# Optimization experiments

Hardware: AMD Instinct MI355X
Metric: run time of the kernel (lower is better)

## Reference

```python
import jax, jax.numpy as jnp
import numpy as np
from jax import lax

BN_EPS = 1e-5


def _zpool(x, axis):
    # stack (mean, max) over `axis` as 2 channels -> [N, 2, A, B]
    return jnp.stack([jnp.mean(x, axis=axis), jnp.max(x, axis=axis)], axis=1)


def _gate(p2, conv_w, conv_b, bn_w, bn_b, bn_rm, bn_rv, i):
    # p2: [N, 2, A, B]; 7x7 conv (2->1, pad 3) + scalar BN + relu + sigmoid
    y = lax.conv_general_dilated(
        p2, conv_w, window_strides=(1, 1), padding=[(3, 3), (3, 3)],
        dimension_numbers=("NCHW", "OIHW", "NCHW"))[:, 0] + conv_b[0]  # [N, A, B]
    y = (y - bn_rm[i]) * lax.rsqrt(bn_rv[i] + BN_EPS) * bn_w[i] + bn_b[i]
    return jax.nn.sigmoid(jnp.maximum(y, 0.0))


def setup_inputs() -> dict:
    key = jax.random.key(0)
    ks = jax.random.split(key, 7)
    N, C, H, W = 256, 2048, 7, 7
    return {
        "x": jax.random.normal(ks[0], (N, C, H, W), dtype=jnp.float32),
        "conv_w": jax.random.normal(ks[1], (1, 2, 7, 7), dtype=jnp.float32) * 0.1,
        "conv_b": jax.random.normal(ks[2], (1,), dtype=jnp.float32) * 0.1,
        "bn_w": jax.random.normal(ks[3], (3,), dtype=jnp.float32),
        "bn_b": jax.random.normal(ks[4], (3,), dtype=jnp.float32),
        "bn_rm": jax.random.normal(ks[5], (3,), dtype=jnp.float32) * 0.1,
        "bn_rv": jax.random.uniform(ks[6], (3,), dtype=jnp.float32),
    }


def reference(x, conv_w, conv_b, bn_w, bn_b, bn_rm, bn_rv):
    # x: [N, C, 7, 7]
    g_hw = _gate(_zpool(x, 1), conv_w, conv_b, bn_w, bn_b, bn_rm, bn_rv, 0)  # [N, 7, 7]
    g_ch = _gate(_zpool(x, 3), conv_w, conv_b, bn_w, bn_b, bn_rm, bn_rv, 1)  # [N, C, 7] indexed by h
    g_cw = _gate(_zpool(x, 2), conv_w, conv_b, bn_w, bn_b, bn_rm, bn_rv, 2)  # [N, C, 7] indexed by w
    gate = (g_hw[:, None, :, :] + g_ch[:, :, :, None] + g_cw[:, :, None, :]) * (1.0 / 3.0)
    return x * gate
```

## Files before the change

kernel.cpp:

```cpp
#include <hip/hip_runtime.h>

#define N_ 256
#define C_ 2048
#define HW_ 49
#define CPB 64
#define NCC 32
#define NCHUNK 8


__global__ __launch_bounds__(256) void k_pool_gate(const float* __restrict__ x,
    const float* __restrict__ cw, const float* __restrict__ cb,
    const float* __restrict__ bnw, const float* __restrict__ bnb,
    const float* __restrict__ bnrm, const float* __restrict__ bnrv,
    float* __restrict__ psum, float* __restrict__ pmax,
    float* __restrict__ gch_g, float* __restrict__ gcw_g) {
  const int bc = blockIdx.x, n = blockIdx.y;
  const int t = threadIdx.x;

  __shared__ __align__(16) float sx[3584];
  __shared__ __align__(16) float pool_lo[4 * 264 * 4];
  __shared__ __align__(16) float pool_hi[4 * 264 * 4];
  __shared__ float part_s[HW_][5];
  __shared__ float part_m[HW_][5];
  __shared__ __align__(16) float s_w[112];

  if (t < 112) {
    int i2w = t / 56, rem = t % 56, p = rem / 8, q = rem % 8;
    s_w[t] = (q < 7) ? cw[i2w * 49 + p * 7 + q] : 0.f;
  }

  float sm = 0.f, mx = -3.4e38f;
  const int hwp = t / 5, sp = t % 5;

  const float4* xv = (const float4*)(x + ((size_t)n * C_ + (size_t)bc * 256) * HW_);
  float4* sv = (float4*)sx;
  #pragma unroll
  for (int pass = 0; pass < 4; ++pass) {
    for (int v = t; v < 784; v += 256) sv[v] = xv[pass * 784 + v];
    __syncthreads();
    if (t < 245) {
      #pragma unroll
      for (int j = 0; j < 13; ++j) {
        int c = sp * 13 + j;
        if (c < CPB) { float a = sx[c * HW_ + hwp]; sm += a; mx = fmaxf(mx, a); }
      }
    }
    for (int i = t; i < 448; i += 256) {
      int lc = i / 7, k = i % 7;
      int base = lc * HW_;
      float s1 = 0.f, m1 = -3.4e38f, s2 = 0.f, m2 = -3.4e38f;
      #pragma unroll
      for (int j = 0; j < 7; ++j) {
        float a = sx[base + k * 7 + j]; s1 += a; m1 = fmaxf(m1, a);
        float b = sx[base + j * 7 + k]; s2 += b; m2 = fmaxf(m2, b);
      }
      int pc = pass * 64 + 3 + lc;
      int kk = k & 3;
      float* pb = (k < 4) ? pool_lo : pool_hi;
      pb[(0 * 264 + pc) * 4 + kk] = s1 * (1.f / 7.f);
      pb[(1 * 264 + pc) * 4 + kk] = m1;
      pb[(2 * 264 + pc) * 4 + kk] = s2 * (1.f / 7.f);
      pb[(3 * 264 + pc) * 4 + kk] = m2;
    }
    __syncthreads();
  }

  if (t < 42) {
    int hc = t / 7, k = t % 7;
    int pc = (hc < 3) ? hc : 259 + (hc - 3);
    int c = bc * 256 - 3 + pc;
    float s1 = 0.f, m1 = 0.f, s2 = 0.f, m2 = 0.f;
    if (c >= 0 && c < C_) {
      m1 = -3.4e38f; m2 = -3.4e38f;
      const float* xp = x + ((size_t)n * C_ + c) * HW_;
      #pragma unroll
      for (int j = 0; j < 7; ++j) {
        float a = xp[k * 7 + j]; s1 += a; m1 = fmaxf(m1, a);
        float b = xp[j * 7 + k]; s2 += b; m2 = fmaxf(m2, b);
      }
      s1 *= (1.f / 7.f); s2 *= (1.f / 7.f);
    }
    int kk = k & 3;
    float* pb = (k < 4) ? pool_lo : pool_hi;
    pb[(0 * 264 + pc) * 4 + kk] = s1;
    pb[(1 * 264 + pc) * 4 + kk] = m1;
    pb[(2 * 264 + pc) * 4 + kk] = s2;
    pb[(3 * 264 + pc) * 4 + kk] = m2;
  }
  if (t < 245) { part_s[hwp][sp] = sm; part_m[hwp][sp] = mx; }
  __syncthreads();

  if (t < HW_) {
    float s2 = 0.f, m2 = -3.4e38f;
    #pragma unroll
    for (int k = 0; k < 5; ++k) { s2 += part_s[t][k]; m2 = fmaxf(m2, part_m[t][k]); }
    size_t o = ((size_t)n * NCHUNK + bc) * HW_ + t;
    psum[o] = s2; pmax[o] = m2;
  }

  const float cb0 = cb[0];
  const float sc1 = bnw[1] * rsqrtf(bnrv[1] + 1e-5f), rm1 = bnrm[1], sh1 = bnb[1];
  const float sc2 = bnw[2] * rsqrtf(bnrv[2] + 1e-5f), rm2 = bnrm[2], sh2 = bnb[2];
  float g0[7] = {0, 0, 0, 0, 0, 0, 0};
  float g1[7] = {0, 0, 0, 0, 0, 0, 0};
  #pragma unroll
  for (int f = 0; f < 4; ++f) {
    const float* Wb = s_w + (f & 1) * 56;
    #pragma unroll
    for (int p = 0; p < 7; ++p) {
      int ri = (f * 264 + t + p) * 4;
      float4 lo4 = *(const float4*)(pool_lo + ri);
      float4 hi4 = *(const float4*)(pool_hi + ri);
      float row[7] = {lo4.x, lo4.y, lo4.z, lo4.w, hi4.x, hi4.y, hi4.z};
      float4 w0 = *(const float4*)(Wb + p * 8);
      float4 w1 = *(const float4*)(Wb + p * 8 + 4);
      float wr[7] = {w0.x, w0.y, w0.z, w0.w, w1.x, w1.y, w1.z};
      #pragma unroll
      for (int q = 0; q < 7; ++q)
        #pragma unroll
        for (int k = 0; k < 7; ++k) {
          int c = k + q - 3;
          if (c >= 0 && c < 7) {
            if (f < 2) g0[k] += row[c] * wr[q];
            else       g1[k] += row[c] * wr[q];
          }
        }
    }
  }
  #pragma unroll
  for (int k = 0; k < 7; ++k) {
    float y0 = (g0[k] + cb0 - rm1) * sc1 + sh1;
    y0 = fmaxf(y0, 0.f);
    sx[t * 7 + k] = 1.f / (1.f + __expf(-y0));
    float y1 = (g1[k] + cb0 - rm2) * sc2 + sh2;
    y1 = fmaxf(y1, 0.f);
    sx[1792 + t * 7 + k] = 1.f / (1.f + __expf(-y1));
  }
  __syncthreads();
  {
    size_t goff = ((size_t)n * C_ + (size_t)bc * 256) * 7;
    const float4* gs = (const float4*)sx;
    float4* d1 = (float4*)(gch_g + goff);
    float4* d2 = (float4*)(gcw_g + goff);
    for (int v = t; v < 896; v += 256) {
      if (v < 448) d1[v] = gs[v];
      else         d2[v - 448] = gs[v];
    }
  }
}

__global__ __launch_bounds__(64) void k_ghw(const float* __restrict__ psum,
                                            const float* __restrict__ pmax,
                                            const float* __restrict__ cw,
                                            const float* __restrict__ cb,
                                            const float* __restrict__ bnw,
                                            const float* __restrict__ bnb,
                                            const float* __restrict__ bnrm,
                                            const float* __restrict__ bnrv,
                                            float* __restrict__ ghw) {
  const int n = blockIdx.x;
  const int t = threadIdx.x;
  __shared__ float p2c[2][13][13];
  __shared__ float s_cw[98];

  for (int i = t; i < 2 * 13 * 13; i += 64) ((float*)p2c)[i] = 0.f;
  for (int i = t; i < 98; i += 64) s_cw[i] = cw[i];
  __syncthreads();

  if (t < HW_) {
    float sm = 0.f, mx = -3.4e38f;
    const float* ps = psum + (size_t)n * NCHUNK * HW_ + t;
    const float* pm = pmax + (size_t)n * NCHUNK * HW_ + t;
    #pragma unroll
    for (int cc = 0; cc < NCHUNK; ++cc) {
      sm += ps[cc * HW_];
      mx = fmaxf(mx, pm[cc * HW_]);
    }
    p2c[0][t / 7 + 3][t % 7 + 3] = sm * (1.f / C_);
    p2c[1][t / 7 + 3][t % 7 + 3] = mx;
  }
  __syncthreads();

  if (t < HW_) {
    int a = t / 7, b = t % 7;
    float y = cb[0];
    #pragma unroll
    for (int i2 = 0; i2 < 2; ++i2)
      #pragma unroll
      for (int p = 0; p < 7; ++p)
        #pragma unroll
        for (int q = 0; q < 7; ++q)
          y += p2c[i2][a + p][b + q] * s_cw[i2 * 49 + p * 7 + q];
    float sc = bnw[0] * rsqrtf(bnrv[0] + 1e-5f);
    y = (y - bnrm[0]) * sc + bnb[0];
    y = fmaxf(y, 0.f);
    ghw[n * HW_ + t] = 1.f / (1.f + __expf(-y));
  }
}

__global__ __launch_bounds__(256) void k_mul(const float* __restrict__ x,
    const float* __restrict__ ghw, const float* __restrict__ gch_g,
    const float* __restrict__ gcw_g, float* __restrict__ out) {
  const int cc = blockIdx.x;
  const int n  = (N_ - 1) - blockIdx.y;
  const int c0 = cc * CPB;
  const int t  = threadIdx.x;

  __shared__ float sg[960];

  {
    const float* g1 = gch_g + ((size_t)n * C_ + c0) * 7;
    const float* g2 = gcw_g + ((size_t)n * C_ + c0) * 7;
    for (int i = t; i < 945; i += 256) {
      float v;
      if (i < 448)      v = g1[i];
      else if (i < 896) v = g2[i - 448];
      else              v = ghw[n * HW_ + (i - 896)];
      sg[i] = v;
    }
  }
  __syncthreads();
  const float* gch = sg;
  const float* gcw = sg + 448;
  const float* s_ghw = sg + 896;

  const float4* xv = (const float4*)(x + ((size_t)n * C_ + c0) * HW_);
  float4* outv = (float4*)(out + ((size_t)n * C_ + c0) * HW_);
  for (int v = t; v < 784; v += 256) {
    float4 q = xv[v];
    int e0 = v * 4;
    int cj = e0 / 49;
    int hw0 = e0 - cj * 49;
    float r0 = q.x, r1 = q.y, r2 = q.z, r3 = q.w;
    {
      int hw = hw0;
      int cjj = cj + (hw >= 49); hw -= (hw >= 49) ? 49 : 0;
      int h = (hw * 37) >> 8, w2 = hw - h * 7;
      r0 *= (s_ghw[hw] + gch[cjj * 7 + h] + gcw[cjj * 7 + w2]) * (1.f / 3.f);
    }
    {
      int hw = hw0 + 1;
      int cjj = cj + (hw >= 49); hw -= (hw >= 49) ? 49 : 0;
      int h = (hw * 37) >> 8, w2 = hw - h * 7;
      r1 *= (s_ghw[hw] + gch[cjj * 7 + h] + gcw[cjj * 7 + w2]) * (1.f / 3.f);
    }
    {
      int hw = hw0 + 2;
      int cjj = cj + (hw >= 49); hw -= (hw >= 49) ? 49 : 0;
      int h = (hw * 37) >> 8, w2 = hw - h * 7;
      r2 *= (s_ghw[hw] + gch[cjj * 7 + h] + gcw[cjj * 7 + w2]) * (1.f / 3.f);
    }
    {
      int hw = hw0 + 3;
      int cjj = cj + (hw >= 49); hw -= (hw >= 49) ? 49 : 0;
      int h = (hw * 37) >> 8, w2 = hw - h * 7;
      r3 *= (s_ghw[hw] + gch[cjj * 7 + h] + gcw[cjj * 7 + w2]) * (1.f / 3.f);
    }
    outv[v] = make_float4(r0, r1, r2, r3);
  }
}


__global__ __launch_bounds__(256) void k_poolc_fb(const float* __restrict__ x,
                                                  float* __restrict__ psum,
                                                  float* __restrict__ pmax) {
  const int bc = blockIdx.x, n = blockIdx.y;
  const int t = threadIdx.x;
  __shared__ __align__(16) float sx[CPB * HW_];
  __shared__ float part_s[HW_][5];
  __shared__ float part_m[HW_][5];

  float sm = 0.f, mx = -3.4e38f;
  const int hw = t / 5, s = t % 5;

  const float4* xv = (const float4*)(x + ((size_t)n * C_ + (size_t)bc * 256) * HW_);
  #pragma unroll
  for (int pass = 0; pass < 4; ++pass) {
    float4* sv = (float4*)sx;
    for (int v = t; v < 784; v += 256) sv[v] = xv[pass * 784 + v];
    __syncthreads();
    if (t < 245) {
      #pragma unroll
      for (int j = 0; j < 13; ++j) {
        int c = s * 13 + j;
        if (c < CPB) { float a = sx[c * HW_ + hw]; sm += a; mx = fmaxf(mx, a); }
      }
    }
    __syncthreads();
  }
  if (t < 245) { part_s[hw][s] = sm; part_m[hw][s] = mx; }
  __syncthreads();
  if (t < HW_) {
    float s2 = 0.f, m2 = -3.4e38f;
    #pragma unroll
    for (int k = 0; k < 5; ++k) { s2 += part_s[t][k]; m2 = fmaxf(m2, part_m[t][k]); }
    size_t o = ((size_t)n * NCHUNK + bc) * HW_ + t;
    psum[o] = s2; pmax[o] = m2;
  }
}

#define CHB(lc) ((lc) * HW_ + ((lc) >= 3 ? 1 : 0))

__global__ __launch_bounds__(256, 6) void k_main_fb(const float* __restrict__ x,
    const float* __restrict__ ghw,
    const float* __restrict__ cw, const float* __restrict__ cb,
    const float* __restrict__ bnw, const float* __restrict__ bnb,
    const float* __restrict__ bnrm, const float* __restrict__ bnrv,
    float* __restrict__ out) {
  const int cc = blockIdx.x;
  const int n  = (N_ - 1) - blockIdx.y;
  const int c0 = cc * CPB;
  const int t  = threadIdx.x;

  __shared__ __align__(16) float sx[3432];
  __shared__ __align__(16) float pool_lo[1120];
  __shared__ __align__(16) float pool_hi[1120];
  __shared__ float gch[448];
  __shared__ float gcw[448];
  __shared__ __align__(16) float s_w[112];
  __shared__ float s_ghw[49];

  const int conv = t & 1, i2 = (t >> 1) & 1, cl = t >> 2;
  const int bi = 1 + conv;
  const float cb0 = cb[0];
  const float sc_bn = bnw[bi] * rsqrtf(bnrv[bi] + 1e-5f);
  const float rm_bn = bnrm[bi];
  const float sh_bn = bnb[bi];

  if (t < 112) {
    int i2w = t / 56, rem = t % 56, p = rem / 8, q = rem % 8;
    s_w[t] = (q < 7) ? cw[i2w * 49 + p * 7 + q] : 0.f;
  }
  if (t < HW_) s_ghw[t] = ghw[n * HW_ + t];
  for (int i = t; i < 2 * 3 * HW_; i += 256) {
    int side = i / 147, off = i % 147;
    int lc = side ? (67 + off / HW_) : (off / HW_);
    int c = c0 - 3 + lc;
    float vv = 0.f;
    if (c >= 0 && c < C_) vv = x[((size_t)n * C_ + c) * HW_ + off % HW_];
    sx[CHB(lc) + off % HW_] = vv;
  }
  const float4* xv = (const float4*)(x + ((size_t)n * C_ + c0) * HW_);
  float4* sxv = (float4*)(sx + 148);
  for (int v = t; v < 784; v += 256) sxv[v] = xv[v];
  __syncthreads();

  for (int i = t; i < 70 * 7; i += 256) {
    int lc = i / 7, k = i % 7;
    int base = CHB(lc);
    float s1 = 0.f, m1 = -3.4e38f, s2 = 0.f, m2 = -3.4e38f;
    #pragma unroll
    for (int j = 0; j < 7; ++j) {
      float a = sx[base + k * 7 + j]; s1 += a; m1 = fmaxf(m1, a);
      float b = sx[base + j * 7 + k]; s2 += b; m2 = fmaxf(m2, b);
    }
    float* pb = (k < 4) ? pool_lo : pool_hi;
    int kk = k & 3;
    pb[((conv * 0 + 0) * 70 + lc) * 4 + kk + 0 * 280] = 0.f;
    pb[(0 * 70 + lc) * 4 + kk] = s1 * (1.f / 7.f);
    pb[(1 * 70 + lc) * 4 + kk] = m1;
    pb[(2 * 70 + lc) * 4 + kk] = s2 * (1.f / 7.f);
    pb[(3 * 70 + lc) * 4 + kk] = m2;
  }
  __syncthreads();

  {
    const int f = conv * 2 + i2;
    const float* Wb = s_w + i2 * 56;
    float acc[7] = {0.f, 0.f, 0.f, 0.f, 0.f, 0.f, 0.f};
    #pragma unroll
    for (int p = 0; p < 7; ++p) {
      int ri = (f * 70 + cl + p) * 4;
      float4 r0 = *(const float4*)(pool_lo + ri);
      float4 r1 = *(const float4*)(pool_hi + ri);
      float row[7] = {r0.x, r0.y, r0.z, r0.w, r1.x, r1.y, r1.z};
      float4 w0 = *(const float4*)(Wb + p * 8);
      float4 w1 = *(const float4*)(Wb + p * 8 + 4);
      float wr[7] = {w0.x, w0.y, w0.z, w0.w, w1.x, w1.y, w1.z};
      #pragma unroll
      for (int q = 0; q < 7; ++q)
        #pragma unroll
        for (int k = 0; k < 7; ++k) {
          int c = k + q - 3;
          if (c >= 0 && c < 7) acc[k] += row[c] * wr[q];
        }
    }
    float fsum[7];
    #pragma unroll
    for (int k = 0; k < 7; ++k) fsum[k] = acc[k] + __shfl_xor(acc[k], 2, 64);
    if (i2 == 0) {
      float* gp = (conv ? gcw : gch) + cl * 7;
      #pragma unroll
      for (int k = 0; k < 7; ++k) {
        float y = (fsum[k] + cb0 - rm_bn) * sc_bn + sh_bn;
        y = fmaxf(y, 0.f);
        gp[k] = 1.f / (1.f + __expf(-y));
      }
    }
  }
  __syncthreads();

  float4* outv = (float4*)(out + ((size_t)n * C_ + c0) * HW_);
  for (int v = t; v < 784; v += 256) {
    float4 q = sxv[v];
    int e0 = v * 4;
    int cj = e0 / 49;
    int hw0 = e0 - cj * 49;
    float r[4] = {q.x, q.y, q.z, q.w};
    #pragma unroll
    for (int j = 0; j < 4; ++j) {
      int hw = hw0 + j;
      int cjj = cj + (hw >= 49);
      hw -= (hw >= 49) ? 49 : 0;
      int h = (hw * 37) >> 8, w2 = hw - h * 7;
      r[j] *= (s_ghw[hw] + gch[cjj * 7 + h] + gcw[cjj * 7 + w2]) * (1.f / 3.f);
    }
    outv[v] = make_float4(r[0], r[1], r[2], r[3]);
  }
}


extern "C" void kernel_launch(void* const* d_in, const int* in_sizes, int n_in,
                              void* d_out, int out_size, void* d_ws, size_t ws_size,
                              hipStream_t stream) {
  const float* x    = (const float*)d_in[0];
  const float* cw   = (const float*)d_in[1];
  const float* cb   = (const float*)d_in[2];
  const float* bnw  = (const float*)d_in[3];
  const float* bnb  = (const float*)d_in[4];
  const float* bnrm = (const float*)d_in[5];
  const float* bnrv = (const float*)d_in[6];
  float* out = (float*)d_out;

  float* psum  = (float*)d_ws;
  float* pmax  = psum + (size_t)N_ * NCHUNK * HW_;
  float* ghw   = pmax + (size_t)N_ * NCHUNK * HW_;
  float* gch_g = ghw + (size_t)N_ * HW_;
  float* gcw_g = gch_g + (size_t)N_ * C_ * 7;
  size_t need_floats = (size_t)N_ * NCHUNK * HW_ * 2 + (size_t)N_ * HW_
                     + (size_t)N_ * C_ * 7 * 2;

  if (ws_size >= need_floats * sizeof(float)) {
    k_pool_gate<<<dim3(NCHUNK, N_), 256, 0, stream>>>(
        x, cw, cb, bnw, bnb, bnrm, bnrv, psum, pmax, gch_g, gcw_g);
    k_ghw<<<dim3(N_), 64, 0, stream>>>(psum, pmax, cw, cb, bnw, bnb, bnrm, bnrv, ghw);
    k_mul<<<dim3(NCC, N_), 256, 0, stream>>>(x, ghw, gch_g, gcw_g, out);
  } else {
    k_poolc_fb<<<dim3(NCHUNK, N_), 256, 0, stream>>>(x, psum, pmax);
    k_ghw<<<dim3(N_), 64, 0, stream>>>(psum, pmax, cw, cb, bnw, bnb, bnrm, bnrv, ghw);
    k_main_fb<<<dim3(NCC, N_), 256, 0, stream>>>(x, ghw, cw, cb, bnw, bnb, bnrm, bnrv, out);
  }
}
```

Measured before the change: 86.97 us.

## Split pool-gate kernel into 64-channel blocks with halos and per-thread conv split

The first kernel now processes 64 channels per block across 32 chunks per sample instead of 256 channels in 4 sequential passes, loading 3-channel halos into shared memory. Each block uses all 256 threads for the 7x7 conv, one per (channel, conv, input-plane), and combines the two input planes with a lane shuffle. Gates are written straight to global memory without staging through shared memory. The aim is more blocks, fewer barriers and better occupancy. The cost is halo reloads and four times as many partial sums for the hw reduction kernel to read.

Result: slower. 90.30 us (+3.8%).

```diff
diff --git a/kernel.cpp b/kernel.cpp
--- a/kernel.cpp
+++ b/kernel.cpp
@@ -5,113 +5,100 @@
 #define HW_ 49
 #define CPB 64
 #define NCC 32
-#define NCHUNK 8
-
-
-__global__ __launch_bounds__(256) void k_pool_gate(const float* __restrict__ x,
+#define NCHUNK_FB 8
+
+#define CHB(lc) ((lc) * HW_ + ((lc) >= 3 ? 1 : 0))
+
+
+__global__ __launch_bounds__(256) void k_gate(const float* __restrict__ x,
     const float* __restrict__ cw, const float* __restrict__ cb,
     const float* __restrict__ bnw, const float* __restrict__ bnb,
     const float* __restrict__ bnrm, const float* __restrict__ bnrv,
     float* __restrict__ psum, float* __restrict__ pmax,
     float* __restrict__ gch_g, float* __restrict__ gcw_g) {
-  const int bc = blockIdx.x, n = blockIdx.y;
-  const int t = threadIdx.x;
-
-  __shared__ __align__(16) float sx[3584];
-  __shared__ __align__(16) float pool_lo[4 * 264 * 4];
-  __shared__ __align__(16) float pool_hi[4 * 264 * 4];
+  const int cc = blockIdx.x, n = blockIdx.y;
+  const int c0 = cc * CPB;
+  const int t  = threadIdx.x;
+
+  __shared__ __align__(16) float sx[3432];
+  __shared__ __align__(16) float pool_lo[1120];
+  __shared__ __align__(16) float pool_hi[1120];
   __shared__ float part_s[HW_][5];
   __shared__ float part_m[HW_][5];
   __shared__ __align__(16) float s_w[112];
 
+  const int conv = t & 1, i2 = (t >> 1) & 1, cl = t >> 2;
+  const int bi = 1 + conv;
+  const float cb0 = cb[0];
+  const float sc_bn = bnw[bi] * rsqrtf(bnrv[bi] + 1e-5f);
+  const float rm_bn = bnrm[bi];
+  const float sh_bn = bnb[bi];
+
   if (t < 112) {
     int i2w = t / 56, rem = t % 56, p = rem / 8, q = rem % 8;
     s_w[t] = (q < 7) ? cw[i2w * 49 + p * 7 + q] : 0.f;
   }
-
-  float sm = 0.f, mx = -3.4e38f;
-  const int hwp = t / 5, sp = t % 5;
-
-  const float4* xv = (const float4*)(x + ((size_t)n * C_ + (size_t)bc * 256) * HW_);
-  float4* sv = (float4*)sx;
-  #pragma unroll
-  for (int pass = 0; pass < 4; ++pass) {
-    for (int v = t; v < 784; v += 256) sv[v] = xv[pass * 784 + v];
-    __syncthreads();
-    if (t < 245) {
-      #pragma unroll
-      for (int j = 0; j < 13; ++j) {
-        int c = sp * 13 + j;
-        if (c < CPB) { float a = sx[c * HW_ + hwp]; sm += a; mx = fmaxf(mx, a); }
+  for (int i = t; i < 2 * 3 * HW_; i += 256) {
+    int side = i / 147, off = i % 147;
+    int lc = side ? (67 + off / HW_) : (off / HW_);
+    int c = c0 - 3 + lc;
+    float vv = 0.f;
+    if (c >= 0 && c < C_) vv = x[((size_t)n * C_ + c) * HW_ + off % HW_];
+    sx[CHB(lc) + off % HW_] = vv;
+  }
+  const float4* xv = (const float4*)(x + ((size_t)n * C_ + c0) * HW_);
+  float4* sxv = (float4*)(sx + 148);
+  for (int v = t; v < 784; v += 256) sxv[v] = xv[v];
+  __syncthreads();
+
+  for (int i = t; i < 70 * 7; i += 256) {
+    int lc = i / 7, k = i % 7;
+    int base = CHB(lc);
+    float s1 = 0.f, m1 = -3.4e38f, s2 = 0.f, m2 = -3.4e38f;
+    #pragma unroll
+    for (int j = 0; j < 7; ++j) {
+      float a = sx[base + k * 7 + j]; s1 += a; m1 = fmaxf(m1, a);
+      float b = sx[base + j * 7 + k]; s2 += b; m2 = fmaxf(m2, b);
+    }
+    float* pb = (k < 4) ? pool_lo : pool_hi;
+    int kk = k & 3;
+    pb[(0 * 70 + lc) * 4 + kk] = s1 * (1.f / 7.f);
+    pb[(1 * 70 + lc) * 4 + kk] = m1;
+    pb[(2 * 70 + lc) * 4 + kk] = s2 * (1.f / 7.f);
+    pb[(3 * 70 + lc) * 4 + kk] = m2;
+  }
+  if (t < 245) {
+    int hw = t / 5, s = t % 5;
+    float sm = 0.f, mx = -3.4e38f;
+    #pragma unroll
+    for (int j = 0; j < 13; ++j) {
+      int c = s * 13 + j;
+      if (c < CPB) {
+        float a = sx[(c + 3) * HW_ + 1 + hw];
+        sm += a; mx = fmaxf(mx, a);
       }
     }
-    for (int i = t; i < 448; i += 256) {
-      int lc = i / 7, k = i % 7;
-      int base = lc * HW_;
-      float s1 = 0.f, m1 = -3.4e38f, s2 = 0.f, m2 = -3.4e38f;
-      #pragma unroll
-      for (int j = 0; j < 7; ++j) {
-        float a = sx[base + k * 7 + j]; s1 += a; m1 = fmaxf(m1, a);
-        float b = sx[base + j * 7 + k]; s2 += b; m2 = fmaxf(m2, b);
-      }
-      int pc = pass * 64 + 3 + lc;
-      int kk = k & 3;
-      float* pb = (k < 4) ? pool_lo : pool_hi;
-      pb[(0 * 264 + pc) * 4 + kk] = s1 * (1.f / 7.f);
-      pb[(1 * 264 + pc) * 4 + kk] = m1;
-      pb[(2 * 264 + pc) * 4 + kk] = s2 * (1.f / 7.f);
-      pb[(3 * 264 + pc) * 4 + kk] = m2;
-    }
-    __syncthreads();
-  }
-
-  if (t < 42) {
-    int hc = t / 7, k = t % 7;
-    int pc = (hc < 3) ? hc : 259 + (hc - 3);
-    int c = bc * 256 - 3 + pc;
-    float s1 = 0.f, m1 = 0.f, s2 = 0.f, m2 = 0.f;
-    if (c >= 0 && c < C_) {
-      m1 = -3.4e38f; m2 = -3.4e38f;
-      const float* xp = x + ((size_t)n * C_ + c) * HW_;
-      #pragma unroll
-      for (int j = 0; j < 7; ++j) {
-        float a = xp[k * 7 + j]; s1 += a; m1 = fmaxf(m1, a);
-        float b = xp[j * 7 + k]; s2 += b; m2 = fmaxf(m2, b);
-      }
-      s1 *= (1.f / 7.f); s2 *= (1.f / 7.f);
-    }
-    int kk = k & 3;
-    float* pb = (k < 4) ? pool_lo : pool_hi;
-    pb[(0 * 264 + pc) * 4 + kk] = s1;
-    pb[(1 * 264 + pc) * 4 + kk] = m1;
-    pb[(2 * 264 + pc) * 4 + kk] = s2;
-    pb[(3 * 264 + pc) * 4 + kk] = m2;
-  }
-  if (t < 245) { part_s[hwp][sp] = sm; part_m[hwp][sp] = mx; }
+    part_s[hw][s] = sm; part_m[hw][s] = mx;
+  }
   __syncthreads();
 
   if (t < HW_) {
-    float s2 = 0.f, m2 = -3.4e38f;
-    #pragma unroll
-    for (int k = 0; k < 5; ++k) { s2 += part_s[t][k]; m2 = fmaxf(m2, part_m[t][k]); }
-    size_t o = ((size_t)n * NCHUNK + bc) * HW_ + t;
-    psum[o] = s2; pmax[o] = m2;
-  }
-
-  const float cb0 = cb[0];
-  const float sc1 = bnw[1] * rsqrtf(bnrv[1] + 1e-5f), rm1 = bnrm[1], sh1 = bnb[1];
-  const float sc2 = bnw[2] * rsqrtf(bnrv[2] + 1e-5f), rm2 = bnrm[2], sh2 = bnb[2];
-  float g0[7] = {0, 0, 0, 0, 0, 0, 0};
-  float g1[7] = {0, 0, 0, 0, 0, 0, 0};
-  #pragma unroll
-  for (int f = 0; f < 4; ++f) {
-    const float* Wb = s_w + (f & 1) * 56;
+    float sm = 0.f, mx = -3.4e38f;
+    #pragma unroll
+    for (int k = 0; k < 5; ++k) { sm += part_s[t][k]; mx = fmaxf(mx, part_m[t][k]); }
+    size_t o = ((size_t)n * NCC + cc) * HW_ + t;
+    psum[o] = sm; pmax[o] = mx;
+  }
+  {
+    const int f = conv * 2 + i2;
+    const float* Wb = s_w + i2 * 56;
+    float acc[7] = {0.f, 0.f, 0.f, 0.f, 0.f, 0.f, 0.f};
     #pragma unroll
     for (int p = 0; p < 7; ++p) {
-      int ri = (f * 264 + t + p) * 4;
-      float4 lo4 = *(const float4*)(pool_lo + ri);
-      float4 hi4 = *(const float4*)(pool_hi + ri);
-      float row[7] = {lo4.x, lo4.y, lo4.z, lo4.w, hi4.x, hi4.y, hi4.z};
+      int ri = (f * 70 + cl + p) * 4;
+      float4 r0 = *(const float4*)(pool_lo + ri);
+      float4 r1 = *(const float4*)(pool_hi + ri);
+      float row[7] = {r0.x, r0.y, r0.z, r0.w, r1.x, r1.y, r1.z};
       float4 w0 = *(const float4*)(Wb + p * 8);
       float4 w1 = *(const float4*)(Wb + p * 8 + 4);
       float wr[7] = {w0.x, w0.y, w0.z, w0.w, w1.x, w1.y, w1.z};
@@ -120,31 +107,20 @@
         #pragma unroll
         for (int k = 0; k < 7; ++k) {
           int c = k + q - 3;
-          if (c >= 0 && c < 7) {
-            if (f < 2) g0[k] += row[c] * wr[q];
-            else       g1[k] += row[c] * wr[q];
-          }
+          if (c >= 0 && c < 7) acc[k] += row[c] * wr[q];
         }
     }
-  }
-  #pragma unroll
-  for (int k = 0; k < 7; ++k) {
-    float y0 = (g0[k] + cb0 - rm1) * sc1 + sh1;
-    y0 = fmaxf(y0, 0.f);
-    sx[t * 7 + k] = 1.f / (1.f + __expf(-y0));
-    float y1 = (g1[k] + cb0 - rm2) * sc2 + sh2;
-    y1 = fmaxf(y1, 0.f);
-    sx[1792 + t * 7 + k] = 1.f / (1.f + __expf(-y1));
-  }
-  __syncthreads();
-  {
-    size_t goff = ((size_t)n * C_ + (size_t)bc * 256) * 7;
-    const float4* gs = (const float4*)sx;
-    float4* d1 = (float4*)(gch_g + goff);
-    float4* d2 = (float4*)(gcw_g + goff);
-    for (int v = t; v < 896; v += 256) {
-      if (v < 448) d1[v] = gs[v];
-      else         d2[v - 448] = gs[v];
+    float fsum[7];
+    #pragma unroll
+    for (int k = 0; k < 7; ++k) fsum[k] = acc[k] + __shfl_xor(acc[k], 2, 64);
+    if (i2 == 0) {
+      float* gp = (conv ? gcw_g : gch_g) + ((size_t)n * C_ + c0 + cl) * 7;
+      #pragma unroll
+      for (int k = 0; k < 7; ++k) {
+        float y = (fsum[k] + cb0 - rm_bn) * sc_bn + sh_bn;
+        y = fmaxf(y, 0.f);
+        gp[k] = 1.f / (1.f + __expf(-y));
+      }
     }
   }
 }
@@ -157,7 +133,7 @@
                                             const float* __restrict__ bnb,
                                             const float* __restrict__ bnrm,
                                             const float* __restrict__ bnrv,
-                                            float* __restrict__ ghw) {
+                                            float* __restrict__ ghw, int nchunk) {
   const int n = blockIdx.x;
   const int t = threadIdx.x;
   __shared__ float p2c[2][13][13];
@@ -169,10 +145,9 @@
 
   if (t < HW_) {
     float sm = 0.f, mx = -3.4e38f;
-    const float* ps = psum + (size_t)n * NCHUNK * HW_ + t;
-    const float* pm = pmax + (size_t)n * NCHUNK * HW_ + t;
-    #pragma unroll
-    for (int cc = 0; cc < NCHUNK; ++cc) {
+    const float* ps = psum + (size_t)n * nchunk * HW_ + t;
+    const float* pm = pmax + (size_t)n * nchunk * HW_ + t;
+    for (int cc = 0; cc < nchunk; ++cc) {
       sm += ps[cc * HW_];
       mx = fmaxf(mx, pm[cc * HW_]);
     }
@@ -231,32 +206,16 @@
     int e0 = v * 4;
     int cj = e0 / 49;
     int hw0 = e0 - cj * 49;
-    float r0 = q.x, r1 = q.y, r2 = q.z, r3 = q.w;
-    {
-      int hw = hw0;
-      int cjj = cj + (hw >= 49); hw -= (hw >= 49) ? 49 : 0;
+    float r[4] = {q.x, q.y, q.z, q.w};
+    #pragma unroll
+    for (int j = 0; j < 4; ++j) {
+      int hw = hw0 + j;
+      int cjj = cj + (hw >= 49);
+      hw -= (hw >= 49) ? 49 : 0;
       int h = (hw * 37) >> 8, w2 = hw - h * 7;
-      r0 *= (s_ghw[hw] + gch[cjj * 7 + h] + gcw[cjj * 7 + w2]) * (1.f / 3.f);
-    }
-    {
-      int hw = hw0 + 1;
-      int cjj = cj + (hw >= 49); hw -= (hw >= 49) ? 49 : 0;
-      int h = (hw * 37) >> 8, w2 = hw - h * 7;
-      r1 *= (s_ghw[hw] + gch[cjj * 7 + h] + gcw[cjj * 7 + w2]) * (1.f / 3.f);
-    }
-    {
-      int hw = hw0 + 2;
-      int cjj = cj + (hw >= 49); hw -= (hw >= 49) ? 49 : 0;
-      int h = (hw * 37) >> 8, w2 = hw - h * 7;
-      r2 *= (s_ghw[hw] + gch[cjj * 7 + h] + gcw[cjj * 7 + w2]) * (1.f / 3.f);
-    }
-    {
-      int hw = hw0 + 3;
-      int cjj = cj + (hw >= 49); hw -= (hw >= 49) ? 49 : 0;
-      int h = (hw * 37) >> 8, w2 = hw - h * 7;
-      r3 *= (s_ghw[hw] + gch[cjj * 7 + h] + gcw[cjj * 7 + w2]) * (1.f / 3.f);
-    }
-    outv[v] = make_float4(r0, r1, r2, r3);
+      r[j] *= (s_ghw[hw] + gch[cjj * 7 + h] + gcw[cjj * 7 + w2]) * (1.f / 3.f);
+    }
+    outv[v] = make_float4(r[0], r[1], r[2], r[3]);
   }
 }
 
@@ -294,12 +253,10 @@
     float s2 = 0.f, m2 = -3.4e38f;
     #pragma unroll
     for (int k = 0; k < 5; ++k) { s2 += part_s[t][k]; m2 = fmaxf(m2, part_m[t][k]); }
-    size_t o = ((size_t)n * NCHUNK + bc) * HW_ + t;
+    size_t o = ((size_t)n * NCHUNK_FB + bc) * HW_ + t;
     psum[o] = s2; pmax[o] = m2;
   }
 }
-
-#define CHB(lc) ((lc) * HW_ + ((lc) >= 3 ? 1 : 0))
 
 __global__ __launch_bounds__(256, 6) void k_main_fb(const float* __restrict__ x,
     const float* __restrict__ ghw,
@@ -356,7 +313,6 @@
     }
     float* pb = (k < 4) ? pool_lo : pool_hi;
     int kk = k & 3;
-    pb[((conv * 0 + 0) * 70 + lc) * 4 + kk + 0 * 280] = 0.f;
     pb[(0 * 70 + lc) * 4 + kk] = s1 * (1.f / 7.f);
     pb[(1 * 70 + lc) * 4 + kk] = m1;
     pb[(2 * 70 + lc) * 4 + kk] = s2 * (1.f / 7.f);
@@ -418,7 +374,6 @@
     outv[v] = make_float4(r[0], r[1], r[2], r[3]);
   }
 }
-
 
 extern "C" void kernel_launch(void* const* d_in, const int* in_sizes, int n_in,
                               void* d_out, int out_size, void* d_ws, size_t ws_size,
@@ -433,21 +388,24 @@
   float* out = (float*)d_out;
 
   float* psum  = (float*)d_ws;
-  float* pmax  = psum + (size_t)N_ * NCHUNK * HW_;
-  float* ghw   = pmax + (size_t)N_ * NCHUNK * HW_;
+  float* pmax  = psum + (size_t)N_ * NCC * HW_;
+  float* ghw   = pmax + (size_t)N_ * NCC * HW_;
   float* gch_g = ghw + (size_t)N_ * HW_;
   float* gcw_g = gch_g + (size_t)N_ * C_ * 7;
-  size_t need_floats = (size_t)N_ * NCHUNK * HW_ * 2 + (size_t)N_ * HW_
+  size_t need_floats = (size_t)N_ * NCC * HW_ * 2 + (size_t)N_ * HW_
                      + (size_t)N_ * C_ * 7 * 2;
 
   if (ws_size >= need_floats * sizeof(float)) {
-    k_pool_gate<<<dim3(NCHUNK, N_), 256, 0, stream>>>(
+    k_gate<<<dim3(NCC, N_), 256, 0, stream>>>(
         x, cw, cb, bnw, bnb, bnrm, bnrv, psum, pmax, gch_g, gcw_g);
-    k_ghw<<<dim3(N_), 64, 0, stream>>>(psum, pmax, cw, cb, bnw, bnb, bnrm, bnrv, ghw);
+    k_ghw<<<dim3(N_), 64, 0, stream>>>(psum, pmax, cw, cb, bnw, bnb, bnrm, bnrv,
+                                       ghw, NCC);
     k_mul<<<dim3(NCC, N_), 256, 0, stream>>>(x, ghw, gch_g, gcw_g, out);
   } else {
-    k_poolc_fb<<<dim3(NCHUNK, N_), 256, 0, stream>>>(x, psum, pmax);
-    k_ghw<<<dim3(N_), 64, 0, stream>>>(psum, pmax, cw, cb, bnw, bnb, bnrm, bnrv, ghw);
-    k_main_fb<<<dim3(NCC, N_), 256, 0, stream>>>(x, ghw, cw, cb, bnw, bnb, bnrm, bnrv, out);
-  }
-}
+    k_poolc_fb<<<dim3(NCHUNK_FB, N_), 256, 0, stream>>>(x, psum, pmax);
+    k_ghw<<<dim3(N_), 64, 0, stream>>>(psum, pmax, cw, cb, bnw, bnb, bnrm, bnrv,
+                                       ghw, NCHUNK_FB);
+    k_main_fb<<<dim3(NCC, N_), 256, 0, stream>>>(x, ghw, cw, cb, bnw, bnb, bnrm,
+                                                 bnrv, out);
+  }
+}
```
